# Kernel optimization log

Hardware: AMD Instinct MI355X
Metric: run time of the kernel (lower is better)

Reference implementation:

```python
import jax, jax.numpy as jnp
import numpy as np

CHANNELS = [64, 128, 256, 512, 512]
RES = [256, 128, 64, 32, 16]
N = 8          # batch
NQ = 128       # n_quad
NCW = 128      # nc_w (output descriptor size)
GRAD_BOOST = 10.0


def _norm(x):
    # Norm module: per-sample, per-row normalization over last dim; torch std is unbiased (ddof=1)
    m = jnp.mean(x, axis=-1, keepdims=True)
    s = jnp.std(x, axis=-1, ddof=1, keepdims=True)
    return (x - m) / (s + 1e-8)


def _quad(x, w):
    # Quad_module: (M^T @ softmax(grad_boost*w, axis=0))**2, summed over spatial dim
    n, c, h, wd = x.shape
    M = x.reshape(n, c, h * wd)                      # (N, C, HW)
    sm = jax.nn.softmax(w * GRAD_BOOST, axis=0)      # (C, NQ)
    proj = jnp.einsum('nch,co->nho', M, sm)          # (N, HW, NQ)
    return jnp.sum(proj ** 2, axis=1)                # (N, NQ)


def setup_inputs() -> dict:
    key = jax.random.key(0)
    ks = jax.random.split(key, 20)
    inp = {}
    for i, (c, r) in enumerate(zip(CHANNELS, RES)):
        inp[f"x{i}"] = jax.random.normal(ks[i], (N, c, r, r), dtype=jnp.float32)
        # torch init: 5/grad_boost * rand(n_in, n_out) = 0.5 * U[0,1)
        inp[f"w1_{i}"] = 0.5 * jax.random.uniform(ks[5 + i], (c, NQ), dtype=jnp.float32)
    d_in = len(CHANNELS) * NQ
    inp["fc1_w"] = jax.random.normal(ks[10], (d_in, 512), dtype=jnp.float32) * 0.04
    inp["fc1_b"] = jnp.zeros((512,), dtype=jnp.float32)
    inp["fc2_w"] = jax.random.normal(ks[11], (512, 512), dtype=jnp.float32) * 0.04
    inp["fc2_b"] = jnp.zeros((512,), dtype=jnp.float32)
    inp["fc3_w"] = jax.random.normal(ks[12], (512, NCW), dtype=jnp.float32) * 0.04
    inp["fc3_b"] = jnp.zeros((NCW,), dtype=jnp.float32)
    return inp


def reference(x0, x1, x2, x3, x4, w1_0, w1_1, w1_2, w1_3, w1_4,
              fc1_w, fc1_b, fc2_w, fc2_b, fc3_w, fc3_b):
    xs = [x0, x1, x2, x3, x4]
    ws = [w1_0, w1_1, w1_2, w1_3, w1_4]
    feats = [_norm(_quad(x, w)) for x, w in zip(xs, ws)]  # each (N, NQ)
    h = jnp.concatenate(feats, axis=1)                    # (N, 5*NQ)
    h = jax.nn.leaky_relu(_norm(h @ fc1_w + fc1_b), 0.01)
    h = jax.nn.leaky_relu(_norm(h @ fc2_w + fc2_b), 0.01)
    return h @ fc3_w + fc3_b                              # (N, NCW)
```

## Files before the change

kernel.cpp:

```cpp
#include <hip/hip_runtime.h>
#include <hip/hip_bf16.h>
#include <stdint.h>

#define NQ 128
#define NLVL 5

typedef float  floatx4 __attribute__((ext_vector_type(4)));
typedef short  short8  __attribute__((ext_vector_type(8)));

__device__ __forceinline__ uint16_t f2bf(float f) {
    uint32_t u = __builtin_bit_cast(uint32_t, f);
    uint32_t r = u + 0x7FFFu + ((u >> 16) & 1u);
    return (uint16_t)(r >> 16);
}
__device__ __forceinline__ uint32_t pack2(float a, float b) {
    return (uint32_t)f2bf(a) | ((uint32_t)f2bf(b) << 16);
}
__device__ __forceinline__ float bf2f(uint16_t u) {
    return __builtin_bit_cast(float, (uint32_t)u << 16);
}

struct SmParams {
    const float* w[NLVL];
    uint16_t*    smT[NLVL];
    int          C[NLVL];
};

__global__ __launch_bounds__(64) void softmax_kernel(SmParams p) {
    int b   = blockIdx.x;
    int lvl = b >> 7;
    int o   = b & 127;
    int C   = p.C[lvl];
    const float* w = p.w[lvl];
    int lane = threadIdx.x;
    float ev[8];
    int nIter = C >> 6;
    float mx = -1e30f;
    for (int it = 0; it < nIter; ++it) {
        float z = 10.0f * w[(size_t)(it * 64 + lane) * NQ + o];
        ev[it] = z;
        mx = fmaxf(mx, z);
    }
    #pragma unroll
    for (int s = 32; s; s >>= 1) mx = fmaxf(mx, __shfl_xor(mx, s));
    float sum = 0.f;
    for (int it = 0; it < nIter; ++it) { ev[it] = expf(ev[it] - mx); sum += ev[it]; }
    #pragma unroll
    for (int s = 32; s; s >>= 1) sum += __shfl_xor(sum, s);
    float inv = 1.0f / sum;
    uint16_t* dst = p.smT[lvl] + (size_t)o * C;
    for (int it = 0; it < nIter; ++it) dst[it * 64 + lane] = f2bf(ev[it] * inv);
}

struct GramParams { const float* x0; const float* x1; float* g0; float* g1; };

template<int C, int HW, int NS>
__device__ __forceinline__ void gram_body(const float* __restrict__ xb,
                                          float* __restrict__ gb,
                                          int h0, short* lds) {
    constexpr int RF   = C / 64;
    constexpr int CF   = C / 16;
    constexpr int PASS = C / 16;
    constexpr int STR  = 72;

    int t    = threadIdx.x;
    int wv   = t >> 6, lane = t & 63, m = lane & 15, kg = lane >> 4;
    int rrow = t >> 4;
    int rcol = (t & 15) * 4;
    const float* src = xb + (size_t)rrow * HW + rcol + h0;

    floatx4 acc[RF][CF];
    floatx4 zero = {0.f, 0.f, 0.f, 0.f};
    #pragma unroll
    for (int rf = 0; rf < RF; ++rf)
        #pragma unroll
        for (int cf = 0; cf < CF; ++cf) acc[rf][cf] = zero;

    float4 pf[PASS];
    #pragma unroll
    for (int p = 0; p < PASS; ++p) pf[p] = *(const float4*)(src + (size_t)p * 16 * HW);
    #pragma unroll
    for (int p = 0; p < PASS; ++p) {
        uint2 pk = { pack2(pf[p].x, pf[p].y), pack2(pf[p].z, pf[p].w) };
        *(uint2*)&lds[(p * 16 + rrow) * STR + rcol] = pk;
    }

    int cur = 0;
    for (int s = 0; s < NS; ++s) {
        if (s + 1 < NS) {
            const float* s2 = src + (s + 1) * 64;
            #pragma unroll
            for (int p = 0; p < PASS; ++p) pf[p] = *(const float4*)(s2 + (size_t)p * 16 * HW);
        }
        __syncthreads();
        const short* bc = lds + cur * (C * STR);
        #pragma unroll
        for (int ksl = 0; ksl < 2; ++ksl) {
            short8 fr[CF], af[RF];
            #pragma unroll
            for (int f = 0; f < CF; ++f)
                fr[f] = *(const short8*)&bc[(f * 16 + m) * STR + ksl * 32 + kg * 8];
            #pragma unroll
            for (int rf = 0; rf < RF; ++rf)
                af[rf] = *(const short8*)&bc[((wv * RF + rf) * 16 + m) * STR + ksl * 32 + kg * 8];
            #pragma unroll
            for (int rf = 0; rf < RF; ++rf)
                #pragma unroll
                for (int cf = 0; cf < CF; ++cf)
                    acc[rf][cf] = __builtin_amdgcn_mfma_f32_16x16x32_bf16(
                        af[rf], fr[cf], acc[rf][cf], 0, 0, 0);
        }
        if (s + 1 < NS) {
            short* bn = lds + (cur ^ 1) * (C * STR);
            #pragma unroll
            for (int p = 0; p < PASS; ++p) {
                uint2 pk = { pack2(pf[p].x, pf[p].y), pack2(pf[p].z, pf[p].w) };
                *(uint2*)&bn[(p * 16 + rrow) * STR + rcol] = pk;
            }
        }
        cur ^= 1;
    }

    #pragma unroll
    for (int rf = 0; rf < RF; ++rf) {
        int row0 = (wv * RF + rf) * 16 + kg * 4;
        #pragma unroll
        for (int cf = 0; cf < CF; ++cf) {
            int col = cf * 16 + m;
            #pragma unroll
            for (int r = 0; r < 4; ++r)
                atomicAdd(&gb[(size_t)(row0 + r) * C + col], acc[rf][cf][r]);
        }
    }
}

__global__ __launch_bounds__(256) void gram_kernel(GramParams p) {
    __shared__ __align__(16) short lds[2 * 128 * 72];
    int b = blockIdx.x;
    if (b < 512) {
        int n = b >> 6, ch = b & 63;
        gram_body<64, 65536, 16>(p.x0 + (size_t)n * 64 * 65536,
                                 p.g0 + (size_t)n * 64 * 64, ch * 1024, lds);
    } else {
        int b2 = b - 512;
        int n = b2 >> 5, ch = b2 & 31;
        gram_body<128, 16384, 8>(p.x1 + (size_t)n * 128 * 16384,
                                 p.g1 + (size_t)n * 128 * 128, ch * 512, lds);
    }
}

struct SgsParams {
    const float* g0; const float* g1;
    const uint16_t* smT0; const uint16_t* smT1;
    float* quad;
};

template<int C>
__device__ __forceinline__ void sgs_body(const float* __restrict__ g,
                                         const uint16_t* __restrict__ smT,
                                         float* __restrict__ qdst, short* Gt) {
    constexpr int RF  = C / 64;
    constexpr int KSL = C / 32;
    constexpr int STR = C + 8;
    int t = threadIdx.x;
    short* Ghi = Gt;
    short* Glo = Gt + C * STR;
    for (int i = t; i < C * C / 4; i += 256) {
        int row = i / (C / 4);
        int c4  = (i % (C / 4)) * 4;
        float4 v = *(const float4*)(g + (size_t)row * C + c4);
        uint16_t h0 = f2bf(v.x), h1 = f2bf(v.y), h2 = f2bf(v.z), h3 = f2bf(v.w);
        uint2 ph = { (uint32_t)h0 | ((uint32_t)h1 << 16),
                     (uint32_t)h2 | ((uint32_t)h3 << 16) };
        uint2 pl = { pack2(v.x - bf2f(h0), v.y - bf2f(h1)),
                     pack2(v.z - bf2f(h2), v.w - bf2f(h3)) };
        *(uint2*)&Ghi[row * STR + c4] = ph;
        *(uint2*)&Glo[row * STR + c4] = pl;
    }
    __syncthreads();
    int wv = t >> 6, lane = t & 63, m = lane & 15, kg = lane >> 4;
    floatx4 acc[RF][8];
    floatx4 zero = {0.f, 0.f, 0.f, 0.f};
    #pragma unroll
    for (int rf = 0; rf < RF; ++rf)
        #pragma unroll
        for (int ot = 0; ot < 8; ++ot) acc[rf][ot] = zero;

    #pragma unroll
    for (int ksl = 0; ksl < KSL; ++ksl) {
        short8 bf[8];
        #pragma unroll
        for (int ot = 0; ot < 8; ++ot)
            bf[ot] = *(const short8*)(smT + (size_t)(ot * 16 + m) * C + ksl * 32 + kg * 8);
        #pragma unroll
        for (int rf = 0; rf < RF; ++rf) {
            int roff = ((wv * RF + rf) * 16 + m) * STR + ksl * 32 + kg * 8;
            short8 ah = *(const short8*)&Ghi[roff];
            short8 al = *(const short8*)&Glo[roff];
            #pragma unroll
            for (int ot = 0; ot < 8; ++ot) {
                acc[rf][ot] = __builtin_amdgcn_mfma_f32_16x16x32_bf16(ah, bf[ot], acc[rf][ot], 0, 0, 0);
                acc[rf][ot] = __builtin_amdgcn_mfma_f32_16x16x32_bf16(al, bf[ot], acc[rf][ot], 0, 0, 0);
            }
        }
    }
    #pragma unroll
    for (int ot = 0; ot < 8; ++ot) {
        float part = 0.f;
        #pragma unroll
        for (int rf = 0; rf < RF; ++rf) {
            int c0 = (wv * RF + rf) * 16 + kg * 4;
            #pragma unroll
            for (int r = 0; r < 4; ++r) {
                float sv = bf2f(smT[(size_t)(ot * 16 + m) * C + c0 + r]);
                part = fmaf(sv, acc[rf][ot][r], part);
            }
        }
        part += __shfl_xor(part, 16);
        part += __shfl_xor(part, 32);
        if (lane < 16) atomicAdd(qdst + (size_t)(ot * 16 + lane) * 16, part);
    }
}

__global__ __launch_bounds__(256) void sgs_kernel(SgsParams p) {
    __shared__ __align__(16) short Gt[2 * 128 * 136];
    int b = blockIdx.x, lvl = b >> 3, n = b & 7;
    if (lvl == 0)
        sgs_body<64>(p.g0 + (size_t)n * 64 * 64, p.smT0,
                     p.quad + (size_t)n * 128 * 16, Gt);
    else
        sgs_body<128>(p.g1 + (size_t)n * 128 * 128, p.smT1,
                      p.quad + (size_t)(8 + n) * 128 * 16, Gt);
}

struct QuadParams {
    const float*    x[NLVL];
    const uint16_t* smT[NLVL];
    float*          quad;
    int             C[NLVL];
    int             HW[NLVL];
    int             blk_base[NLVL];
};

__global__ __launch_bounds__(256) void quad_kernel(QuadParams p) {
    __shared__ __align__(16) short At[64 * 40];
    __shared__ __align__(16) short Bt[128 * 40];

    int bid = blockIdx.x;
    int lvl = 0;
    #pragma unroll
    for (int l = 1; l < 3; ++l) if (bid >= p.blk_base[l]) lvl = l;
    int rel = bid - p.blk_base[lvl];
    int n   = rel & 7;
    int ht  = rel >> 3;
    int C   = p.C[lvl];
    int HW  = p.HW[lvl];
    int h0  = ht * 64;

    const float*    xb  = p.x[lvl] + (size_t)n * C * HW + h0;
    const uint16_t* smT = p.smT[lvl];

    int t    = threadIdx.x;
    int wave = t >> 6;
    int lane = t & 63;
    int m    = lane & 15;
    int kg   = lane >> 4;

    floatx4 acc[4][2];
    floatx4 zero = {0.f, 0.f, 0.f, 0.f};
    #pragma unroll
    for (int i = 0; i < 4; ++i)
        #pragma unroll
        for (int j = 0; j < 2; ++j) acc[i][j] = zero;

    int c_l = (t & 15) * 2;
    int h_l = (t >> 4) * 4;

    for (int c0 = 0; c0 < C; c0 += 32) {
        const float* s1 = xb + (size_t)(c0 + c_l) * HW + h_l;
        float4 a4 = *(const float4*)s1;
        float4 b4 = *(const float4*)(s1 + HW);
        #pragma unroll
        for (int j = 0; j < 4; ++j) {
            uint32_t pk = (uint32_t)f2bf(((const float*)&a4)[j]) |
                          ((uint32_t)f2bf(((const float*)&b4)[j]) << 16);
            *(uint32_t*)&At[(h_l + j) * 40 + c_l] = pk;
        }
        #pragma unroll
        for (int it = 0; it < 2; ++it) {
            int idx  = it * 256 + t;
            int o    = idx >> 2;
            int part = idx & 3;
            uint4 v = *(const uint4*)(smT + (size_t)o * C + c0 + part * 8);
            *(uint4*)&Bt[o * 40 + part * 8] = v;
        }
        __syncthreads();

        short8 af[4];
        #pragma unroll
        for (int mt = 0; mt < 4; ++mt)
            af[mt] = *(const short8*)&At[(mt * 16 + m) * 40 + kg * 8];
        short8 bfr[2];
        #pragma unroll
        for (int ot = 0; ot < 2; ++ot)
            bfr[ot] = *(const short8*)&Bt[((wave * 2 + ot) * 16 + m) * 40 + kg * 8];
        #pragma unroll
        for (int mt = 0; mt < 4; ++mt)
            #pragma unroll
            for (int ot = 0; ot < 2; ++ot)
                acc[mt][ot] = __builtin_amdgcn_mfma_f32_16x16x32_bf16(
                    af[mt], bfr[ot], acc[mt][ot], 0, 0, 0);
        __syncthreads();
    }

    float* qbase = p.quad + (size_t)((lvl + 2) * 8 + n) * 128 * 16;
    #pragma unroll
    for (int ot = 0; ot < 2; ++ot) {
        float part = 0.f;
        #pragma unroll
        for (int mt = 0; mt < 4; ++mt)
            #pragma unroll
            for (int r = 0; r < 4; ++r) {
                float v = acc[mt][ot][r];
                part = fmaf(v, v, part);
            }
        part += __shfl_xor(part, 16);
        part += __shfl_xor(part, 32);
        if (lane < 16) {
            int o = (wave * 2 + ot) * 16 + lane;
            atomicAdd(qbase + (size_t)o * 16, part);
        }
    }
}

__device__ __forceinline__ float block_sum512(float v, float* red8, int t) {
    #pragma unroll
    for (int s = 32; s; s >>= 1) v += __shfl_xor(v, s);
    __syncthreads();
    if ((t & 63) == 0) red8[t >> 6] = v;
    __syncthreads();
    float tot = 0.f;
    #pragma unroll
    for (int i = 0; i < 8; ++i) tot += red8[i];
    return tot;
}

__global__ __launch_bounds__(512) void head_kernel(
    const float* __restrict__ quad,
    const float* __restrict__ fc1_w, const float* __restrict__ fc1_b,
    const float* __restrict__ fc2_w, const float* __restrict__ fc2_b,
    const float* __restrict__ fc3_w, const float* __restrict__ fc3_b,
    float* __restrict__ out) {
    __shared__ float feat[640];
    __shared__ float hbuf[512];
    __shared__ float red8[8];
    __shared__ float stats[10];
    int n = blockIdx.x;
    int t = threadIdx.x;

    for (int idx = t; idx < 640; idx += 512) {
        int lvl = idx >> 7, o = idx & 127;
        feat[idx] = quad[((size_t)(lvl * 8 + n) * 128 + o) * 16];
    }
    __syncthreads();
    if (t < 5) {
        float s = 0.f;
        for (int i = 0; i < 128; ++i) s += feat[t * 128 + i];
        float mean = s * (1.f / 128.f);
        float v = 0.f;
        for (int i = 0; i < 128; ++i) { float d = feat[t * 128 + i] - mean; v += d * d; }
        stats[t]     = mean;
        stats[5 + t] = sqrtf(v * (1.f / 127.f)) + 1e-8f;
    }
    __syncthreads();
    for (int idx = t; idx < 640; idx += 512) {
        int lvl = idx >> 7;
        feat[idx] = (feat[idx] - stats[lvl]) / stats[5 + lvl];
    }
    __syncthreads();

    float acc = fc1_b[t];
    #pragma unroll 8
    for (int i = 0; i < 640; ++i) acc = fmaf(feat[i], fc1_w[(size_t)i * 512 + t], acc);
    float mean = block_sum512(acc, red8, t) * (1.f / 512.f);
    float d    = acc - mean;
    float var  = block_sum512(d * d, red8, t) * (1.f / 511.f);
    float nv   = d / (sqrtf(var) + 1e-8f);
    __syncthreads();
    hbuf[t] = nv > 0.f ? nv : 0.01f * nv;
    __syncthreads();

    float acc2 = fc2_b[t];
    #pragma unroll 8
    for (int i = 0; i < 512; ++i) acc2 = fmaf(hbuf[i], fc2_w[(size_t)i * 512 + t], acc2);
    mean = block_sum512(acc2, red8, t) * (1.f / 512.f);
    d    = acc2 - mean;
    var  = block_sum512(d * d, red8, t) * (1.f / 511.f);
    nv   = d / (sqrtf(var) + 1e-8f);
    __syncthreads();
    hbuf[t] = nv > 0.f ? nv : 0.01f * nv;
    __syncthreads();

    if (t < 128) {
        float acc3 = fc3_b[t];
        #pragma unroll 8
        for (int i = 0; i < 512; ++i) acc3 = fmaf(hbuf[i], fc3_w[(size_t)i * 128 + t], acc3);
        out[(size_t)n * 128 + t] = acc3;
    }
}

extern "C" void kernel_launch(void* const* d_in, const int* in_sizes, int n_in,
                              void* d_out, int out_size, void* d_ws, size_t ws_size,
                              hipStream_t stream) {
    static const int Cs[NLVL]   = {64, 128, 256, 512, 512};
    static const int RESs[NLVL] = {256, 128, 64, 32, 16};

    const float* x[NLVL];
    const float* w[NLVL];
    for (int i = 0; i < NLVL; ++i) {
        x[i] = (const float*)d_in[2 * i];
        w[i] = (const float*)d_in[2 * i + 1];
    }
    const float* fc1_w = (const float*)d_in[10];
    const float* fc1_b = (const float*)d_in[11];
    const float* fc2_w = (const float*)d_in[12];
    const float* fc2_b = (const float*)d_in[13];
    const float* fc3_w = (const float*)d_in[14];
    const float* fc3_b = (const float*)d_in[15];

    uint16_t* smT_base = (uint16_t*)d_ws;
    int smOff[NLVL];
    int off = 0;
    for (int i = 0; i < NLVL; ++i) { smOff[i] = off; off += Cs[i] * NQ; }
    size_t smBytes = (size_t)off * sizeof(uint16_t);
    float* quad = (float*)((char*)d_ws + smBytes);
    size_t quadFloats = (size_t)NLVL * 8 * NQ * 16;
    float* g0 = quad + quadFloats;
    float* g1 = g0 + (size_t)8 * 64 * 64;
    size_t zeroBytes = (quadFloats + (size_t)8 * 64 * 64 + (size_t)8 * 128 * 128) * sizeof(float);

    SmParams sp;
    for (int i = 0; i < NLVL; ++i) {
        sp.w[i]   = w[i];
        sp.smT[i] = smT_base + smOff[i];
        sp.C[i]   = Cs[i];
    }
    softmax_kernel<<<NLVL * NQ, 64, 0, stream>>>(sp);

    hipMemsetAsync(quad, 0, zeroBytes, stream);

    GramParams gp;
    gp.x0 = x[0]; gp.x1 = x[1]; gp.g0 = g0; gp.g1 = g1;
    gram_kernel<<<768, 256, 0, stream>>>(gp);

    QuadParams qp;
    int base = 0;
    for (int i = 0; i < 3; ++i) {
        int lvl = i + 2;
        qp.x[i]   = x[lvl];
        qp.smT[i] = smT_base + smOff[lvl];
        qp.C[i]   = Cs[lvl];
        qp.HW[i]  = RESs[lvl] * RESs[lvl];
        qp.blk_base[i] = base;
        base += (RESs[lvl] * RESs[lvl] / 64) * 8;
    }
    for (int i = 3; i < NLVL; ++i) {
        qp.x[i] = nullptr; qp.smT[i] = nullptr;
        qp.C[i] = 0; qp.HW[i] = 0; qp.blk_base[i] = 0x7fffffff;
    }
    qp.quad = quad;
    quad_kernel<<<base, 256, 0, stream>>>(qp);

    SgsParams ssp;
    ssp.g0 = g0; ssp.g1 = g1;
    ssp.smT0 = smT_base + smOff[0];
    ssp.smT1 = smT_base + smOff[1];
    ssp.quad = quad;
    sgs_kernel<<<16, 256, 0, stream>>>(ssp);

    head_kernel<<<8, 512, 0, stream>>>(quad, fc1_w, fc1_b, fc2_w, fc2_b,
                                       fc3_w, fc3_b, (float*)d_out);
}
```

Before: 461.9 us.

## Split MLP head into three wider-parallel kernels with split-K reductions

Replaces the single 8-block head kernel with three kernels (fc1, fc2, fc3). Each kernel spreads output columns across many blocks and splits K across waves, reducing partial sums through shared memory, and each layer's norm and leaky-relu is fused into the next layer's kernel. The aim is to cut the long serial latency of 8 blocks streaming all the FC weights. In exchange it adds two kernel launches and intermediate round trips through global memory, and the normalisation stats are recomputed redundantly in every block.

```diff
diff --git a/kernel.cpp b/kernel.cpp
--- a/kernel.cpp
+++ b/kernel.cpp
@@ -333,79 +333,133 @@
     }
 }
 
-__device__ __forceinline__ float block_sum512(float v, float* red8, int t) {
-    #pragma unroll
-    for (int s = 32; s; s >>= 1) v += __shfl_xor(v, s);
-    __syncthreads();
-    if ((t & 63) == 0) red8[t >> 6] = v;
-    __syncthreads();
-    float tot = 0.f;
-    #pragma unroll
-    for (int i = 0; i < 8; ++i) tot += red8[i];
-    return tot;
-}
-
-__global__ __launch_bounds__(512) void head_kernel(
-    const float* __restrict__ quad,
-    const float* __restrict__ fc1_w, const float* __restrict__ fc1_b,
-    const float* __restrict__ fc2_w, const float* __restrict__ fc2_b,
-    const float* __restrict__ fc3_w, const float* __restrict__ fc3_b,
-    float* __restrict__ out) {
+
+__global__ __launch_bounds__(256) void hfc1_kernel(
+    const float* __restrict__ quad, const float* __restrict__ w,
+    const float* __restrict__ b, float* __restrict__ h1) {
     __shared__ float feat[640];
-    __shared__ float hbuf[512];
-    __shared__ float red8[8];
     __shared__ float stats[10];
-    int n = blockIdx.x;
+    __shared__ float part[256];
+    int blk = blockIdx.x;
+    int n = blk >> 3, c8 = blk & 7;
     int t = threadIdx.x;
-
-    for (int idx = t; idx < 640; idx += 512) {
-        int lvl = idx >> 7, o = idx & 127;
-        feat[idx] = quad[((size_t)(lvl * 8 + n) * 128 + o) * 16];
-    }
-    __syncthreads();
-    if (t < 5) {
-        float s = 0.f;
-        for (int i = 0; i < 128; ++i) s += feat[t * 128 + i];
+    for (int idx = t; idx < 640; idx += 256) {
+        int L = idx >> 7, o = idx & 127;
+        feat[idx] = quad[((size_t)(L * 8 + n) * 128 + o) * 16];
+    }
+    __syncthreads();
+    int wv = t >> 6, lane = t & 63;
+    for (int L = wv; L < 5; L += 4) {
+        float a = feat[L * 128 + lane], c = feat[L * 128 + 64 + lane];
+        float s = a + c;
+        #pragma unroll
+        for (int sh = 32; sh; sh >>= 1) s += __shfl_xor(s, sh);
         float mean = s * (1.f / 128.f);
-        float v = 0.f;
-        for (int i = 0; i < 128; ++i) { float d = feat[t * 128 + i] - mean; v += d * d; }
-        stats[t]     = mean;
-        stats[5 + t] = sqrtf(v * (1.f / 127.f)) + 1e-8f;
-    }
-    __syncthreads();
-    for (int idx = t; idx < 640; idx += 512) {
-        int lvl = idx >> 7;
-        feat[idx] = (feat[idx] - stats[lvl]) / stats[5 + lvl];
-    }
-    __syncthreads();
-
-    float acc = fc1_b[t];
+        float d0 = a - mean, d1 = c - mean;
+        float v = d0 * d0 + d1 * d1;
+        #pragma unroll
+        for (int sh = 32; sh; sh >>= 1) v += __shfl_xor(v, sh);
+        if (lane == 0) {
+            stats[L]     = mean;
+            stats[5 + L] = 1.f / (sqrtf(v * (1.f / 127.f)) + 1e-8f);
+        }
+    }
+    __syncthreads();
+    for (int idx = t; idx < 640; idx += 256) {
+        int L = idx >> 7;
+        feat[idx] = (feat[idx] - stats[L]) * stats[5 + L];
+    }
+    __syncthreads();
+
+    int o = c8 * 64 + lane;
+    float acc = 0.f;
+    const float* wc = w + o;
+    int k0 = wv * 160;
     #pragma unroll 8
-    for (int i = 0; i < 640; ++i) acc = fmaf(feat[i], fc1_w[(size_t)i * 512 + t], acc);
-    float mean = block_sum512(acc, red8, t) * (1.f / 512.f);
-    float d    = acc - mean;
-    float var  = block_sum512(d * d, red8, t) * (1.f / 511.f);
-    float nv   = d / (sqrtf(var) + 1e-8f);
-    __syncthreads();
-    hbuf[t] = nv > 0.f ? nv : 0.01f * nv;
-    __syncthreads();
-
-    float acc2 = fc2_b[t];
+    for (int k = k0; k < k0 + 160; ++k) acc = fmaf(feat[k], wc[(size_t)k * 512], acc);
+    part[t] = acc;
+    __syncthreads();
+    if (t < 64) {
+        float r = part[t] + part[t + 64] + part[t + 128] + part[t + 192];
+        h1[(size_t)n * 512 + c8 * 64 + t] = r + b[c8 * 64 + t];
+    }
+}
+
+__device__ __forceinline__ void norm_leaky_512(float* buf, float* red, int t) {
+    float a = buf[t], c = buf[t + 256];
+    float s = a + c;
+    #pragma unroll
+    for (int sh = 32; sh; sh >>= 1) s += __shfl_xor(s, sh);
+    if ((t & 63) == 0) red[t >> 6] = s;
+    __syncthreads();
+    float mean = (red[0] + red[1] + red[2] + red[3]) * (1.f / 512.f);
+    float d0 = a - mean, d1 = c - mean;
+    float v = d0 * d0 + d1 * d1;
+    #pragma unroll
+    for (int sh = 32; sh; sh >>= 1) v += __shfl_xor(v, sh);
+    __syncthreads();
+    if ((t & 63) == 0) red[t >> 6] = v;
+    __syncthreads();
+    float inv = 1.f / (sqrtf((red[0] + red[1] + red[2] + red[3]) * (1.f / 511.f)) + 1e-8f);
+    float n0 = d0 * inv, n1 = d1 * inv;
+    buf[t]       = n0 > 0.f ? n0 : 0.01f * n0;
+    buf[t + 256] = n1 > 0.f ? n1 : 0.01f * n1;
+    __syncthreads();
+}
+
+__global__ __launch_bounds__(256) void hfc2_kernel(
+    const float* __restrict__ h1, const float* __restrict__ w,
+    const float* __restrict__ b, float* __restrict__ h2) {
+    __shared__ float buf[512];
+    __shared__ float red[4];
+    __shared__ float part[256];
+    int blk = blockIdx.x;
+    int n = blk >> 3, c8 = blk & 7;
+    int t = threadIdx.x;
+    buf[t]       = h1[(size_t)n * 512 + t];
+    buf[t + 256] = h1[(size_t)n * 512 + t + 256];
+    __syncthreads();
+    norm_leaky_512(buf, red, t);
+    int wv = t >> 6, lane = t & 63;
+    int o = c8 * 64 + lane;
+    float acc = 0.f;
+    const float* wc = w + o;
+    int k0 = wv * 128;
     #pragma unroll 8
-    for (int i = 0; i < 512; ++i) acc2 = fmaf(hbuf[i], fc2_w[(size_t)i * 512 + t], acc2);
-    mean = block_sum512(acc2, red8, t) * (1.f / 512.f);
-    d    = acc2 - mean;
-    var  = block_sum512(d * d, red8, t) * (1.f / 511.f);
-    nv   = d / (sqrtf(var) + 1e-8f);
-    __syncthreads();
-    hbuf[t] = nv > 0.f ? nv : 0.01f * nv;
-    __syncthreads();
-
-    if (t < 128) {
-        float acc3 = fc3_b[t];
-        #pragma unroll 8
-        for (int i = 0; i < 512; ++i) acc3 = fmaf(hbuf[i], fc3_w[(size_t)i * 128 + t], acc3);
-        out[(size_t)n * 128 + t] = acc3;
+    for (int k = k0; k < k0 + 128; ++k) acc = fmaf(buf[k], wc[(size_t)k * 512], acc);
+    part[t] = acc;
+    __syncthreads();
+    if (t < 64) {
+        float r = part[t] + part[t + 64] + part[t + 128] + part[t + 192];
+        h2[(size_t)n * 512 + c8 * 64 + t] = r + b[c8 * 64 + t];
+    }
+}
+
+__global__ __launch_bounds__(256) void hfc3_kernel(
+    const float* __restrict__ h2, const float* __restrict__ w,
+    const float* __restrict__ b, float* __restrict__ out) {
+    __shared__ float buf[512];
+    __shared__ float red[4];
+    __shared__ float part[256];
+    int blk = blockIdx.x;
+    int n = blk >> 1, c2 = blk & 1;
+    int t = threadIdx.x;
+    buf[t]       = h2[(size_t)n * 512 + t];
+    buf[t + 256] = h2[(size_t)n * 512 + t + 256];
+    __syncthreads();
+    norm_leaky_512(buf, red, t);
+    int wv = t >> 6, lane = t & 63;
+    int o = c2 * 64 + lane;
+    float acc = 0.f;
+    const float* wc = w + o;
+    int k0 = wv * 128;
+    #pragma unroll 8
+    for (int k = k0; k < k0 + 128; ++k) acc = fmaf(buf[k], wc[(size_t)k * 128], acc);
+    part[t] = acc;
+    __syncthreads();
+    if (t < 64) {
+        out[(size_t)n * 128 + c2 * 64 + t] =
+            part[t] + part[t + 64] + part[t + 128] + part[t + 192] + b[c2 * 64 + t];
     }
 }
 
@@ -437,6 +491,8 @@
     size_t quadFloats = (size_t)NLVL * 8 * NQ * 16;
     float* g0 = quad + quadFloats;
     float* g1 = g0 + (size_t)8 * 64 * 64;
+    float* h1 = g1 + (size_t)8 * 128 * 128;
+    float* h2 = h1 + (size_t)8 * 512;
     size_t zeroBytes = (quadFloats + (size_t)8 * 64 * 64 + (size_t)8 * 128 * 128) * sizeof(float);
 
     SmParams sp;
@@ -478,6 +534,7 @@
     ssp.quad = quad;
     sgs_kernel<<<16, 256, 0, stream>>>(ssp);
 
-    head_kernel<<<8, 512, 0, stream>>>(quad, fc1_w, fc1_b, fc2_w, fc2_b,
-                                       fc3_w, fc3_b, (float*)d_out);
-}
+    hfc1_kernel<<<64, 256, 0, stream>>>(quad, fc1_w, fc1_b, h1);
+    hfc2_kernel<<<64, 256, 0, stream>>>(h1, fc2_w, fc2_b, h2);
+    hfc3_kernel<<<16, 256, 0, stream>>>(h2, fc3_w, fc3_b, (float*)d_out);
+}
```

Result: faster. 391.1 us (-15.3%).
